# Kernel optimization log

Measured on AMD Instinct MI355X. Metric: run time of the kernel, lower is better.

## Reference

```python
import jax, jax.numpy as jnp
import numpy as np

GRID_SIZE = 5
SPLINE_ORDER = 3
N_COEFFS = GRID_SIZE + SPLINE_ORDER  # 8
N_KNOTS = N_COEFFS + SPLINE_ORDER    # 11
GRID_RANGE = 5.0
# extended knot grid: linspace(-9, 9, 11) for the defaults
_lo = -GRID_RANGE - (SPLINE_ORDER - 1) * 2.0 * GRID_RANGE / GRID_SIZE
_hi = GRID_RANGE + (SPLINE_ORDER - 1) * 2.0 * GRID_RANGE / GRID_SIZE
GRID = jnp.asarray(np.linspace(_lo, _hi, N_KNOTS), dtype=jnp.float32)


def _bspline_basis(x):
    # x: (B, I) -> basis: (B, I, N_COEFFS) via Cox-de Boor recursion
    xe = x[..., None]  # (B, I, 1)
    # order-1 (piecewise-constant) basis over the 10 knot intervals
    bases = ((xe >= GRID[:-1]) & (xe < GRID[1:])).astype(x.dtype)  # (B, I, 10)
    for k in range(1, SPLINE_ORDER):
        n = N_KNOTS - k - 1  # number of bases at this order
        g_i = GRID[:n]
        g_ik = GRID[k:k + n]
        g_i1 = GRID[1:n + 1]
        g_ik1 = GRID[k + 1:k + 1 + n]
        d1 = g_ik - g_i
        d2 = g_ik1 - g_i1
        left = jnp.where(d1 > 1e-8, (xe - g_i) / jnp.where(d1 > 1e-8, d1, 1.0), 0.0) * bases[..., :n]
        right = jnp.where(d2 > 1e-8, (g_ik1 - xe) / jnp.where(d2 > 1e-8, d2, 1.0), 0.0) * bases[..., 1:n + 1]
        bases = left + right
    return bases  # (B, I, 8)


def setup_inputs() -> dict:
    key = jax.random.key(0)
    k1, k2, k3 = jax.random.split(key, 3)
    B, I, O = 8192, 1024, 1024
    x = jax.random.normal(k1, (B, I), dtype=jnp.float32)
    base_weight = jax.random.normal(k2, (O, I), dtype=jnp.float32) * 0.1
    spline_weight = jax.random.normal(k3, (O, I, N_COEFFS), dtype=jnp.float32) * 0.1
    return {"x": x, "base_weight": base_weight, "spline_weight": spline_weight}


def reference(x, base_weight, spline_weight):
    base_out = jnp.einsum('bi,oi->bo', jax.nn.silu(x), base_weight)
    basis = _bspline_basis(x)  # (B, I, 8)
    spline_out = jnp.einsum('bin,oin->bo', basis, spline_weight)
    return base_out + spline_out
```

## Files before the change

### kernel.cpp

```cpp
#include <hip/hip_runtime.h>
#include <hip/hip_bf16.h>

#define B_DIM 8192
#define I_DIM 1024
#define O_DIM 1024
#define K_DIM 9216

#define BM 256
#define BN 128
#define BK 64
#define NKT (K_DIM / BK)

typedef unsigned short ushort_t;
typedef __attribute__((ext_vector_type(8))) short short8;
typedef __attribute__((ext_vector_type(4))) float f32x4;

#define MFMA(a, b, c) __builtin_amdgcn_mfma_f32_16x16x32_bf16((a), (b), (c), 0, 0, 0)

__device__ __forceinline__ ushort_t f2bf(float f) {
    unsigned u = __float_as_uint(f);
    unsigned r = 0x7fffu + ((u >> 16) & 1u);
    return (ushort_t)((u + r) >> 16);
}

__device__ __forceinline__ void llds16(const ushort_t* g, ushort_t* l) {
    __builtin_amdgcn_global_load_lds(
        (const __attribute__((address_space(1))) unsigned int*)g,
        (__attribute__((address_space(3))) unsigned int*)l,
        16, 0, 0);
}

__global__ __launch_bounds__(256) void expand_w_kernel(
        const float* __restrict__ bw, const float* __restrict__ sw,
        ushort_t* __restrict__ Wf) {
    int idx = blockIdx.x * 256 + threadIdx.x;
    int o = idx >> 9;
    int i = (idx & 511) << 1;
    ushort_t* out = Wf + (size_t)o * K_DIM + i;
    const float* bp = bw + ((size_t)o << 10) + i;
    *(unsigned*)out = (unsigned)f2bf(bp[0]) | ((unsigned)f2bf(bp[1]) << 16);
    const float* sp = sw + (((size_t)o << 10) + i) * 8;
    float v[16];
    #pragma unroll
    for (int n = 0; n < 16; ++n) v[n] = sp[n];
    #pragma unroll
    for (int n = 0; n < 8; ++n)
        *(unsigned*)(out + (size_t)(n + 1) * 1024) =
            (unsigned)f2bf(v[n]) | ((unsigned)f2bf(v[8 + n]) << 16);
}

__global__ __launch_bounds__(256) void expand_a_kernel(
        const float* __restrict__ x, ushort_t* __restrict__ Af) {
    int idx = blockIdx.x * 256 + threadIdx.x;
    int b = idx >> 9;
    int i = (idx & 511) << 1;
    const float* xp = x + ((size_t)b << 10) + i;
    float x0 = xp[0], x1 = xp[1];
    ushort_t* out = Af + (size_t)b * K_DIM + i;
    float s0 = x0 / (1.0f + __expf(-x0));
    float s1 = x1 / (1.0f + __expf(-x1));
    *(unsigned*)out = (unsigned)f2bf(s0) | ((unsigned)f2bf(s1) << 16);
    float t0 = (x0 + 9.0f) * (1.0f / 1.8f);
    float t1 = (x1 + 9.0f) * (1.0f / 1.8f);
    float fj0 = floorf(t0), fj1 = floorf(t1);
    int j0 = (int)fj0, j1 = (int)fj1;
    float u0 = t0 - fj0, u1 = t1 - fj1;
    float p0 = 0.5f * (1.f - u0) * (1.f - u0);
    float p1 = 0.5f * (-2.f * u0 * u0 + 2.f * u0 + 1.f);
    float p2 = 0.5f * u0 * u0;
    float q0 = 0.5f * (1.f - u1) * (1.f - u1);
    float q1 = 0.5f * (-2.f * u1 * u1 + 2.f * u1 + 1.f);
    float q2 = 0.5f * u1 * u1;
    #pragma unroll
    for (int n = 0; n < 8; ++n) {
        float v0 = (n == j0 - 2) ? p0 : (n == j0 - 1) ? p1 : (n == j0) ? p2 : 0.f;
        float v1 = (n == j1 - 2) ? q0 : (n == j1 - 1) ? q1 : (n == j1) ? q2 : 0.f;
        *(unsigned*)(out + (size_t)(n + 1) * 1024) =
            (unsigned)f2bf(v0) | ((unsigned)f2bf(v1) << 16);
    }
}

__global__ __launch_bounds__(512, 1) void gemm_bt(
        const ushort_t* __restrict__ Af,
        const ushort_t* __restrict__ Wf,
        float* __restrict__ out) {
    __shared__ __align__(16) ushort_t As[3][BM * BK];
    __shared__ __align__(16) ushort_t Bs[3][BN * BK];

    const int tid = threadIdx.x;

    const int orig = blockIdx.x;
    const int wgid = (orig & 7) * 32 + (orig >> 3);
    const int bm = wgid >> 3;
    const int bn = wgid & 7;
    const int mBase = bm * BM, nBase = bn * BN;

    const int lane = tid & 63;
    const int w = tid >> 6;
    const int wr = (w >> 1) * 64, wc = (w & 1) * 64;
    const int fr = lane & 15;
    const int kg = lane >> 4;

    const int srow = tid >> 3;
    const int scolE = (((tid & 7) ^ (srow & 7)) << 3);
    const int sdst = (tid & ~63) * 8;

    auto stageA = [&](int t, int buf, int rnd) {
        const ushort_t* g = Af + (size_t)(mBase + rnd * 64 + srow) * K_DIM
                               + (size_t)t * BK + scolE;
        llds16(g, &As[buf][rnd * 4096 + sdst]);
    };
    auto stageB = [&](int t, int buf, int rnd) {
        const ushort_t* g = Wf + (size_t)(nBase + rnd * 64 + srow) * K_DIM
                               + (size_t)t * BK + scolE;
        llds16(g, &Bs[buf][rnd * 4096 + sdst]);
    };

    int offA[4][2], offB[4][2];
    #pragma unroll
    for (int m = 0; m < 4; ++m) {
        int row = wr + m * 16 + fr;
        #pragma unroll
        for (int kk = 0; kk < 2; ++kk)
            offA[m][kk] = row * BK + (((kk * 4 + kg) ^ (row & 7)) << 3);
    }
    #pragma unroll
    for (int n = 0; n < 4; ++n) {
        int row = wc + n * 16 + fr;
        #pragma unroll
        for (int kk = 0; kk < 2; ++kk)
            offB[n][kk] = row * BK + (((kk * 4 + kg) ^ (row & 7)) << 3);
    }

    f32x4 acc[4][4];
    #pragma unroll
    for (int m = 0; m < 4; ++m)
        #pragma unroll
        for (int n = 0; n < 4; ++n) acc[m][n] = (f32x4){0.f, 0.f, 0.f, 0.f};

    stageA(0, 0, 0); stageA(0, 0, 1); stageA(0, 0, 2); stageA(0, 0, 3);
    stageB(0, 0, 0); stageB(0, 0, 1);
    stageA(1, 1, 0); stageA(1, 1, 1); stageA(1, 1, 2); stageA(1, 1, 3);
    stageB(1, 1, 0); stageB(1, 1, 1);

    int cur = 0;
    for (int t = 0; t < NKT; ++t) {
        if (t + 1 < NKT) asm volatile("s_waitcnt vmcnt(6)" ::: "memory");
        else             asm volatile("s_waitcnt vmcnt(0)" ::: "memory");
        __builtin_amdgcn_s_barrier();

        const int pf = (cur >= 1) ? cur - 1 : 2;
        const bool dopf = (t + 2 < NKT);
        const ushort_t* A_ = As[cur];
        const ushort_t* B_ = Bs[cur];

        short8 a[4][2], b[2][2];
        #pragma unroll
        for (int m = 0; m < 4; ++m) {
            a[m][0] = *(const short8*)&A_[offA[m][0]];
            a[m][1] = *(const short8*)&A_[offA[m][1]];
        }
        #pragma unroll
        for (int n = 0; n < 2; ++n) {
            b[n][0] = *(const short8*)&B_[offB[n][0]];
            b[n][1] = *(const short8*)&B_[offB[n][1]];
        }
        if (dopf) { stageA(t + 2, pf, 0); stageA(t + 2, pf, 1); stageA(t + 2, pf, 2); }
        asm volatile("s_waitcnt lgkmcnt(0)" ::: "memory");
        __builtin_amdgcn_sched_barrier(0);
        __builtin_amdgcn_s_setprio(1);
        #pragma unroll
        for (int m = 0; m < 4; ++m)
            #pragma unroll
            for (int n = 0; n < 2; ++n) {
                acc[m][n] = MFMA(a[m][0], b[n][0], acc[m][n]);
                acc[m][n] = MFMA(a[m][1], b[n][1], acc[m][n]);
            }
        __builtin_amdgcn_s_setprio(0);
        __builtin_amdgcn_s_barrier();

        short8 b2[2][2];
        #pragma unroll
        for (int n = 0; n < 2; ++n) {
            b2[n][0] = *(const short8*)&B_[offB[2 + n][0]];
            b2[n][1] = *(const short8*)&B_[offB[2 + n][1]];
        }
        if (dopf) { stageA(t + 2, pf, 3); stageB(t + 2, pf, 0); stageB(t + 2, pf, 1); }
        asm volatile("s_waitcnt lgkmcnt(0)" ::: "memory");
        __builtin_amdgcn_sched_barrier(0);
        __builtin_amdgcn_s_setprio(1);
        #pragma unroll
        for (int m = 0; m < 4; ++m)
            #pragma unroll
            for (int n = 0; n < 2; ++n) {
                acc[m][2 + n] = MFMA(a[m][0], b2[n][0], acc[m][2 + n]);
                acc[m][2 + n] = MFMA(a[m][1], b2[n][1], acc[m][2 + n]);
            }
        __builtin_amdgcn_s_setprio(0);

        cur = (cur + 1 == 3) ? 0 : cur + 1;
    }

    const int orow = (lane >> 4) * 4;
    const int ocol = lane & 15;
    #pragma unroll
    for (int m = 0; m < 4; ++m)
        #pragma unroll
        for (int n = 0; n < 4; ++n) {
            size_t base = (size_t)(mBase + wr + m * 16 + orow) * O_DIM
                        + (nBase + wc + n * 16 + ocol);
            #pragma unroll
            for (int r = 0; r < 4; ++r)
                out[base + (size_t)r * O_DIM] = acc[m][n][r];
        }
}

extern "C" void kernel_launch(void* const* d_in, const int* in_sizes, int n_in,
                              void* d_out, int out_size, void* d_ws, size_t ws_size,
                              hipStream_t stream) {
    const float* x  = (const float*)d_in[0];
    const float* bw = (const float*)d_in[1];
    const float* sw = (const float*)d_in[2];
    float* out = (float*)d_out;

    ushort_t* Wf = (ushort_t*)d_ws;
    ushort_t* Af = Wf + (size_t)O_DIM * K_DIM;

    expand_w_kernel<<<(O_DIM * I_DIM / 2) / 256, 256, 0, stream>>>(bw, sw, Wf);
    expand_a_kernel<<<(B_DIM * I_DIM / 2) / 256, 256, 0, stream>>>(x, Af);
    gemm_bt<<<(B_DIM / BM) * (O_DIM / BN), 512, 0, stream>>>(Af, Wf, out);
}
```

Before: 171.5 us.

## Use 256x256 GEMM tiles with split-K over two halves and reduction

Grows the GEMM block tile from 256x128 to 256x256, which raises per-block data reuse and gives each warp 8x4 accumulators. To keep the GPU occupied with fewer tiles, K is split in two when the workspace is large enough. Each split writes a partial result and a separate kernel adds them. The LDS pipeline is reworked to double-buffer B and triple-buffer A, with four MFMA phases per k-tile. The cost is an extra 32MB partial write, a reduction pass, and higher register pressure.

```diff
diff --git a/kernel.cpp b/kernel.cpp
--- a/kernel.cpp
+++ b/kernel.cpp
@@ -7,9 +7,8 @@
 #define K_DIM 9216
 
 #define BM 256
-#define BN 128
+#define BN 256
 #define BK 64
-#define NKT (K_DIM / BK)
 
 typedef unsigned short ushort_t;
 typedef __attribute__((ext_vector_type(8))) short short8;
@@ -83,21 +82,26 @@
 __global__ __launch_bounds__(512, 1) void gemm_bt(
         const ushort_t* __restrict__ Af,
         const ushort_t* __restrict__ Wf,
-        float* __restrict__ out) {
+        float* __restrict__ out, float* __restrict__ part1,
+        int kTiles) {
     __shared__ __align__(16) ushort_t As[3][BM * BK];
-    __shared__ __align__(16) ushort_t Bs[3][BN * BK];
+    __shared__ __align__(16) ushort_t Bs[2][BN * BK];
 
     const int tid = threadIdx.x;
 
+    const int nwg = gridDim.x;
     const int orig = blockIdx.x;
-    const int wgid = (orig & 7) * 32 + (orig >> 3);
-    const int bm = wgid >> 3;
-    const int bn = wgid & 7;
+    const int wgid = (orig & 7) * (nwg >> 3) + (orig >> 3);
+    const int split = wgid >> 7;
+    const int bm = (wgid & 127) >> 2;
+    const int bn = wgid & 3;
     const int mBase = bm * BM, nBase = bn * BN;
+    const size_t kOff = (size_t)split * kTiles * BK;
 
     const int lane = tid & 63;
     const int w = tid >> 6;
-    const int wr = (w >> 1) * 64, wc = (w & 1) * 64;
+    const int wr = (w >> 2) * 128;
+    const int wc = (w & 3) * 64;
     const int fr = lane & 15;
     const int kg = lane >> 4;
 
@@ -107,112 +111,162 @@
 
     auto stageA = [&](int t, int buf, int rnd) {
         const ushort_t* g = Af + (size_t)(mBase + rnd * 64 + srow) * K_DIM
-                               + (size_t)t * BK + scolE;
+                               + kOff + (size_t)t * BK + scolE;
         llds16(g, &As[buf][rnd * 4096 + sdst]);
     };
     auto stageB = [&](int t, int buf, int rnd) {
         const ushort_t* g = Wf + (size_t)(nBase + rnd * 64 + srow) * K_DIM
-                               + (size_t)t * BK + scolE;
+                               + kOff + (size_t)t * BK + scolE;
         llds16(g, &Bs[buf][rnd * 4096 + sdst]);
     };
 
-    int offA[4][2], offB[4][2];
-    #pragma unroll
-    for (int m = 0; m < 4; ++m) {
-        int row = wr + m * 16 + fr;
-        #pragma unroll
-        for (int kk = 0; kk < 2; ++kk)
-            offA[m][kk] = row * BK + (((kk * 4 + kg) ^ (row & 7)) << 3);
-    }
-    #pragma unroll
-    for (int n = 0; n < 4; ++n) {
-        int row = wc + n * 16 + fr;
-        #pragma unroll
-        for (int kk = 0; kk < 2; ++kk)
-            offB[n][kk] = row * BK + (((kk * 4 + kg) ^ (row & 7)) << 3);
-    }
-
-    f32x4 acc[4][4];
-    #pragma unroll
-    for (int m = 0; m < 4; ++m)
+    const int swz0 = ((kg ^ (fr & 7)) << 3);
+    const int swz1 = (((4 + kg) ^ (fr & 7)) << 3);
+
+    f32x4 acc[8][4];
+    #pragma unroll
+    for (int m = 0; m < 8; ++m)
         #pragma unroll
         for (int n = 0; n < 4; ++n) acc[m][n] = (f32x4){0.f, 0.f, 0.f, 0.f};
 
+    stageB(0, 0, 0); stageB(0, 0, 1); stageB(0, 0, 2); stageB(0, 0, 3);
     stageA(0, 0, 0); stageA(0, 0, 1); stageA(0, 0, 2); stageA(0, 0, 3);
-    stageB(0, 0, 0); stageB(0, 0, 1);
     stageA(1, 1, 0); stageA(1, 1, 1); stageA(1, 1, 2); stageA(1, 1, 3);
-    stageB(1, 1, 0); stageB(1, 1, 1);
-
-    int cur = 0;
-    for (int t = 0; t < NKT; ++t) {
-        if (t + 1 < NKT) asm volatile("s_waitcnt vmcnt(6)" ::: "memory");
-        else             asm volatile("s_waitcnt vmcnt(0)" ::: "memory");
+
+    int ca = 0;
+    for (int t = 0; t < kTiles; ++t) {
+        if (t + 1 < kTiles) asm volatile("s_waitcnt vmcnt(4)" ::: "memory");
+        else                asm volatile("s_waitcnt vmcnt(0)" ::: "memory");
         __builtin_amdgcn_s_barrier();
 
-        const int pf = (cur >= 1) ? cur - 1 : 2;
-        const bool dopf = (t + 2 < NKT);
-        const ushort_t* A_ = As[cur];
-        const ushort_t* B_ = Bs[cur];
-
-        short8 a[4][2], b[2][2];
+        const int pa = (ca >= 1) ? ca - 1 : 2;
+        const ushort_t* A_ = As[ca];
+        const ushort_t* B_ = Bs[t & 1];
+
+        if (t + 1 < kTiles) {
+            stageB(t + 1, (t + 1) & 1, 0); stageB(t + 1, (t + 1) & 1, 1);
+            stageB(t + 1, (t + 1) & 1, 2); stageB(t + 1, (t + 1) & 1, 3);
+        }
+        short8 b[4][2];
         #pragma unroll
-        for (int m = 0; m < 4; ++m) {
-            a[m][0] = *(const short8*)&A_[offA[m][0]];
-            a[m][1] = *(const short8*)&A_[offA[m][1]];
-        }
-        #pragma unroll
-        for (int n = 0; n < 2; ++n) {
-            b[n][0] = *(const short8*)&B_[offB[n][0]];
-            b[n][1] = *(const short8*)&B_[offB[n][1]];
-        }
-        if (dopf) { stageA(t + 2, pf, 0); stageA(t + 2, pf, 1); stageA(t + 2, pf, 2); }
-        asm volatile("s_waitcnt lgkmcnt(0)" ::: "memory");
-        __builtin_amdgcn_sched_barrier(0);
-        __builtin_amdgcn_s_setprio(1);
-        #pragma unroll
-        for (int m = 0; m < 4; ++m)
-            #pragma unroll
-            for (int n = 0; n < 2; ++n) {
-                acc[m][n] = MFMA(a[m][0], b[n][0], acc[m][n]);
-                acc[m][n] = MFMA(a[m][1], b[n][1], acc[m][n]);
-            }
-        __builtin_amdgcn_s_setprio(0);
+        for (int n = 0; n < 4; ++n) {
+            int brow = (wc + n * 16 + fr) * BK;
+            b[n][0] = *(const short8*)&B_[brow + swz0];
+            b[n][1] = *(const short8*)&B_[brow + swz1];
+        }
+        {
+            short8 a[2][2];
+            #pragma unroll
+            for (int m = 0; m < 2; ++m) {
+                int arow = (wr + m * 16 + fr) * BK;
+                a[m][0] = *(const short8*)&A_[arow + swz0];
+                a[m][1] = *(const short8*)&A_[arow + swz1];
+            }
+            asm volatile("s_waitcnt lgkmcnt(0)" ::: "memory");
+            __builtin_amdgcn_sched_barrier(0);
+            __builtin_amdgcn_s_setprio(1);
+            #pragma unroll
+            for (int m = 0; m < 2; ++m)
+                #pragma unroll
+                for (int n = 0; n < 4; ++n) {
+                    acc[m][n] = MFMA(a[m][0], b[n][0], acc[m][n]);
+                    acc[m][n] = MFMA(a[m][1], b[n][1], acc[m][n]);
+                }
+            __builtin_amdgcn_s_setprio(0);
+        }
+
+        if (t + 2 < kTiles) {
+            stageA(t + 2, pa, 0); stageA(t + 2, pa, 1);
+            stageA(t + 2, pa, 2); stageA(t + 2, pa, 3);
+        }
+        {
+            short8 a[2][2];
+            #pragma unroll
+            for (int m = 0; m < 2; ++m) {
+                int arow = (wr + (2 + m) * 16 + fr) * BK;
+                a[m][0] = *(const short8*)&A_[arow + swz0];
+                a[m][1] = *(const short8*)&A_[arow + swz1];
+            }
+            asm volatile("s_waitcnt lgkmcnt(0)" ::: "memory");
+            __builtin_amdgcn_sched_barrier(0);
+            __builtin_amdgcn_s_setprio(1);
+            #pragma unroll
+            for (int m = 0; m < 2; ++m)
+                #pragma unroll
+                for (int n = 0; n < 4; ++n) {
+                    acc[2 + m][n] = MFMA(a[m][0], b[n][0], acc[2 + m][n]);
+                    acc[2 + m][n] = MFMA(a[m][1], b[n][1], acc[2 + m][n]);
+                }
+            __builtin_amdgcn_s_setprio(0);
+        }
         __builtin_amdgcn_s_barrier();
 
-        short8 b2[2][2];
-        #pragma unroll
-        for (int n = 0; n < 2; ++n) {
-            b2[n][0] = *(const short8*)&B_[offB[2 + n][0]];
-            b2[n][1] = *(const short8*)&B_[offB[2 + n][1]];
-        }
-        if (dopf) { stageA(t + 2, pf, 3); stageB(t + 2, pf, 0); stageB(t + 2, pf, 1); }
-        asm volatile("s_waitcnt lgkmcnt(0)" ::: "memory");
-        __builtin_amdgcn_sched_barrier(0);
-        __builtin_amdgcn_s_setprio(1);
-        #pragma unroll
-        for (int m = 0; m < 4; ++m)
-            #pragma unroll
-            for (int n = 0; n < 2; ++n) {
-                acc[m][2 + n] = MFMA(a[m][0], b2[n][0], acc[m][2 + n]);
-                acc[m][2 + n] = MFMA(a[m][1], b2[n][1], acc[m][2 + n]);
-            }
-        __builtin_amdgcn_s_setprio(0);
-
-        cur = (cur + 1 == 3) ? 0 : cur + 1;
+        {
+            short8 a[2][2];
+            #pragma unroll
+            for (int m = 0; m < 2; ++m) {
+                int arow = (wr + (4 + m) * 16 + fr) * BK;
+                a[m][0] = *(const short8*)&A_[arow + swz0];
+                a[m][1] = *(const short8*)&A_[arow + swz1];
+            }
+            asm volatile("s_waitcnt lgkmcnt(0)" ::: "memory");
+            __builtin_amdgcn_sched_barrier(0);
+            __builtin_amdgcn_s_setprio(1);
+            #pragma unroll
+            for (int m = 0; m < 2; ++m)
+                #pragma unroll
+                for (int n = 0; n < 4; ++n) {
+                    acc[4 + m][n] = MFMA(a[m][0], b[n][0], acc[4 + m][n]);
+                    acc[4 + m][n] = MFMA(a[m][1], b[n][1], acc[4 + m][n]);
+                }
+            __builtin_amdgcn_s_setprio(0);
+        }
+
+        {
+            short8 a[2][2];
+            #pragma unroll
+            for (int m = 0; m < 2; ++m) {
+                int arow = (wr + (6 + m) * 16 + fr) * BK;
+                a[m][0] = *(const short8*)&A_[arow + swz0];
+                a[m][1] = *(const short8*)&A_[arow + swz1];
+            }
+            asm volatile("s_waitcnt lgkmcnt(0)" ::: "memory");
+            __builtin_amdgcn_sched_barrier(0);
+            __builtin_amdgcn_s_setprio(1);
+            #pragma unroll
+            for (int m = 0; m < 2; ++m)
+                #pragma unroll
+                for (int n = 0; n < 4; ++n) {
+                    acc[6 + m][n] = MFMA(a[m][0], b[n][0], acc[6 + m][n]);
+                    acc[6 + m][n] = MFMA(a[m][1], b[n][1], acc[6 + m][n]);
+                }
+            __builtin_amdgcn_s_setprio(0);
+        }
+
+        ca = (ca + 1 == 3) ? 0 : ca + 1;
     }
 
+    float* obase = split ? part1 : out;
     const int orow = (lane >> 4) * 4;
     const int ocol = lane & 15;
     #pragma unroll
-    for (int m = 0; m < 4; ++m)
+    for (int m = 0; m < 8; ++m)
         #pragma unroll
         for (int n = 0; n < 4; ++n) {
             size_t base = (size_t)(mBase + wr + m * 16 + orow) * O_DIM
                         + (nBase + wc + n * 16 + ocol);
             #pragma unroll
             for (int r = 0; r < 4; ++r)
-                out[base + (size_t)r * O_DIM] = acc[m][n][r];
-        }
+                obase[base + (size_t)r * O_DIM] = acc[m][n][r];
+        }
+}
+
+__global__ __launch_bounds__(256) void reduce_kernel(
+        float* __restrict__ out, const float* __restrict__ p1) {
+    int i = blockIdx.x * 256 + threadIdx.x;
+    f32x4 a = ((const f32x4*)out)[i];
+    f32x4 b = ((const f32x4*)p1)[i];
+    ((f32x4*)out)[i] = a + b;
 }
 
 extern "C" void kernel_launch(void* const* d_in, const int* in_sizes, int n_in,
@@ -223,10 +277,20 @@
     const float* sw = (const float*)d_in[2];
     float* out = (float*)d_out;
 
+    const size_t nW = (size_t)O_DIM * K_DIM;
+    const size_t nA = (size_t)B_DIM * K_DIM;
     ushort_t* Wf = (ushort_t*)d_ws;
-    ushort_t* Af = Wf + (size_t)O_DIM * K_DIM;
+    ushort_t* Af = Wf + nW;
+    float* part1 = (float*)(Af + nA);
+    const size_t need = (nW + nA) * 2 + (size_t)B_DIM * O_DIM * 4;
+
+    const int nsplit = (ws_size >= need) ? 2 : 1;
+    const int kTiles = (K_DIM / BK) / nsplit;
+    const int nwg = 128 * nsplit;
 
     expand_w_kernel<<<(O_DIM * I_DIM / 2) / 256, 256, 0, stream>>>(bw, sw, Wf);
     expand_a_kernel<<<(B_DIM * I_DIM / 2) / 256, 256, 0, stream>>>(x, Af);
-    gemm_bt<<<(B_DIM / BM) * (O_DIM / BN), 512, 0, stream>>>(Af, Wf, out);
-}
+    gemm_bt<<<nwg, 512, 0, stream>>>(Af, Wf, out, part1, kTiles);
+    if (nsplit == 2)
+        reduce_kernel<<<(B_DIM * O_DIM / 4) / 256, 256, 0, stream>>>(out, part1);
+}
```

Result: slower. 220.7 us (+28.7%).

## Load weight tile fragments directly to registers and drop B shared-memory staging

Applied to the files above, without the earlier changes.

The GEMM no longer stages the weight (B) tile through LDS. Each wave loads its B fragments straight from global memory into double-buffered registers one k-tile ahead, while the A tile stays on the triple-buffered global-to-LDS path. The block index mapping also becomes column-major over M, so consecutive blocks share the same weight columns, and the occupancy hint of 1 is dropped from launch bounds. This cuts LDS use and LDS reads, but adds register pressure and makes uncoalesced 16-byte global loads for B that depend on cache hits.

```diff
diff --git a/kernel.cpp b/kernel.cpp
--- a/kernel.cpp
+++ b/kernel.cpp
@@ -80,19 +80,18 @@
     }
 }
 
-__global__ __launch_bounds__(512, 1) void gemm_bt(
+__global__ __launch_bounds__(512) void gemm_bt(
         const ushort_t* __restrict__ Af,
         const ushort_t* __restrict__ Wf,
         float* __restrict__ out) {
     __shared__ __align__(16) ushort_t As[3][BM * BK];
-    __shared__ __align__(16) ushort_t Bs[3][BN * BK];
 
     const int tid = threadIdx.x;
 
     const int orig = blockIdx.x;
     const int wgid = (orig & 7) * 32 + (orig >> 3);
-    const int bm = wgid >> 3;
-    const int bn = wgid & 7;
+    const int bn = wgid >> 5;
+    const int bm = wgid & 31;
     const int mBase = bm * BM, nBase = bn * BN;
 
     const int lane = tid & 63;
@@ -105,32 +104,27 @@
     const int scolE = (((tid & 7) ^ (srow & 7)) << 3);
     const int sdst = (tid & ~63) * 8;
 
-    auto stageA = [&](int t, int buf, int rnd) {
-        const ushort_t* g = Af + (size_t)(mBase + rnd * 64 + srow) * K_DIM
-                               + (size_t)t * BK + scolE;
-        llds16(g, &As[buf][rnd * 4096 + sdst]);
+    auto stageA = [&](int t, int buf) {
+        #pragma unroll
+        for (int rnd = 0; rnd < 4; ++rnd) {
+            const ushort_t* g = Af + (size_t)(mBase + rnd * 64 + srow) * K_DIM
+                                   + (size_t)t * BK + scolE;
+            llds16(g, &As[buf][rnd * 4096 + sdst]);
+        }
     };
-    auto stageB = [&](int t, int buf, int rnd) {
-        const ushort_t* g = Wf + (size_t)(nBase + rnd * 64 + srow) * K_DIM
-                               + (size_t)t * BK + scolE;
-        llds16(g, &Bs[buf][rnd * 4096 + sdst]);
+
+    const ushort_t* Wbase = Wf + (size_t)(nBase + wc + fr) * K_DIM + kg * 8;
+    auto bload = [&](int t, short8 (&b)[4][2]) {
+        #pragma unroll
+        for (int n = 0; n < 4; ++n)
+            #pragma unroll
+            for (int kk = 0; kk < 2; ++kk)
+                b[n][kk] = *(const short8*)(Wbase + (size_t)n * 16 * K_DIM
+                                                  + (size_t)t * BK + kk * 32);
     };
 
-    int offA[4][2], offB[4][2];
-    #pragma unroll
-    for (int m = 0; m < 4; ++m) {
-        int row = wr + m * 16 + fr;
-        #pragma unroll
-        for (int kk = 0; kk < 2; ++kk)
-            offA[m][kk] = row * BK + (((kk * 4 + kg) ^ (row & 7)) << 3);
-    }
-    #pragma unroll
-    for (int n = 0; n < 4; ++n) {
-        int row = wc + n * 16 + fr;
-        #pragma unroll
-        for (int kk = 0; kk < 2; ++kk)
-            offB[n][kk] = row * BK + (((kk * 4 + kg) ^ (row & 7)) << 3);
-    }
+    const int swz0 = ((kg ^ (fr & 7)) << 3);
+    const int swz1 = (((4 + kg) ^ (fr & 7)) << 3);
 
     f32x4 acc[4][4];
     #pragma unroll
@@ -138,67 +132,71 @@
         #pragma unroll
         for (int n = 0; n < 4; ++n) acc[m][n] = (f32x4){0.f, 0.f, 0.f, 0.f};
 
-    stageA(0, 0, 0); stageA(0, 0, 1); stageA(0, 0, 2); stageA(0, 0, 3);
-    stageB(0, 0, 0); stageB(0, 0, 1);
-    stageA(1, 1, 0); stageA(1, 1, 1); stageA(1, 1, 2); stageA(1, 1, 3);
-    stageB(1, 1, 0); stageB(1, 1, 1);
-
-    int cur = 0;
-    for (int t = 0; t < NKT; ++t) {
-        if (t + 1 < NKT) asm volatile("s_waitcnt vmcnt(6)" ::: "memory");
-        else             asm volatile("s_waitcnt vmcnt(0)" ::: "memory");
+    short8 bA[4][2], bB[4][2];
+
+    bload(0, bA);
+    __builtin_amdgcn_sched_barrier(0);
+    stageA(0, 0);
+    stageA(1, 1);
+
+    int ca = 0;
+    auto tile = [&](int t, short8 (&bc)[4][2], short8 (&bnx)[4][2]) {
+        if (t == NKT - 1) asm volatile("s_waitcnt vmcnt(0)" ::: "memory");
+        else              asm volatile("s_waitcnt vmcnt(4)" ::: "memory");
         __builtin_amdgcn_s_barrier();
 
-        const int pf = (cur >= 1) ? cur - 1 : 2;
-        const bool dopf = (t + 2 < NKT);
-        const ushort_t* A_ = As[cur];
-        const ushort_t* B_ = Bs[cur];
-
-        short8 a[4][2], b[2][2];
-        #pragma unroll
-        for (int m = 0; m < 4; ++m) {
-            a[m][0] = *(const short8*)&A_[offA[m][0]];
-            a[m][1] = *(const short8*)&A_[offA[m][1]];
-        }
-        #pragma unroll
-        for (int n = 0; n < 2; ++n) {
-            b[n][0] = *(const short8*)&B_[offB[n][0]];
-            b[n][1] = *(const short8*)&B_[offB[n][1]];
-        }
-        if (dopf) { stageA(t + 2, pf, 0); stageA(t + 2, pf, 1); stageA(t + 2, pf, 2); }
+        const ushort_t* A_ = As[ca];
+        const int pa = (ca >= 1) ? ca - 1 : 2;
+
+        if (t + 1 < NKT) bload(t + 1, bnx);
+        __builtin_amdgcn_sched_barrier(0);
+        short8 a1[2][2];
+        #pragma unroll
+        for (int i = 0; i < 2; ++i) {
+            int arow = (wr + i * 16 + fr) * BK;
+            a1[i][0] = *(const short8*)&A_[arow + swz0];
+            a1[i][1] = *(const short8*)&A_[arow + swz1];
+        }
         asm volatile("s_waitcnt lgkmcnt(0)" ::: "memory");
         __builtin_amdgcn_sched_barrier(0);
         __builtin_amdgcn_s_setprio(1);
         #pragma unroll
-        for (int m = 0; m < 4; ++m)
-            #pragma unroll
-            for (int n = 0; n < 2; ++n) {
-                acc[m][n] = MFMA(a[m][0], b[n][0], acc[m][n]);
-                acc[m][n] = MFMA(a[m][1], b[n][1], acc[m][n]);
+        for (int i = 0; i < 2; ++i)
+            #pragma unroll
+            for (int n = 0; n < 4; ++n) {
+                acc[i][n] = MFMA(a1[i][0], bc[n][0], acc[i][n]);
+                acc[i][n] = MFMA(a1[i][1], bc[n][1], acc[i][n]);
             }
         __builtin_amdgcn_s_setprio(0);
         __builtin_amdgcn_s_barrier();
 
-        short8 b2[2][2];
-        #pragma unroll
-        for (int n = 0; n < 2; ++n) {
-            b2[n][0] = *(const short8*)&B_[offB[2 + n][0]];
-            b2[n][1] = *(const short8*)&B_[offB[2 + n][1]];
-        }
-        if (dopf) { stageA(t + 2, pf, 3); stageB(t + 2, pf, 0); stageB(t + 2, pf, 1); }
+        if (t + 2 < NKT) stageA(t + 2, pa);
+        __builtin_amdgcn_sched_barrier(0);
+        short8 a2[2][2];
+        #pragma unroll
+        for (int i = 0; i < 2; ++i) {
+            int arow = (wr + (2 + i) * 16 + fr) * BK;
+            a2[i][0] = *(const short8*)&A_[arow + swz0];
+            a2[i][1] = *(const short8*)&A_[arow + swz1];
+        }
         asm volatile("s_waitcnt lgkmcnt(0)" ::: "memory");
         __builtin_amdgcn_sched_barrier(0);
         __builtin_amdgcn_s_setprio(1);
         #pragma unroll
-        for (int m = 0; m < 4; ++m)
-            #pragma unroll
-            for (int n = 0; n < 2; ++n) {
-                acc[m][2 + n] = MFMA(a[m][0], b2[n][0], acc[m][2 + n]);
-                acc[m][2 + n] = MFMA(a[m][1], b2[n][1], acc[m][2 + n]);
+        for (int i = 0; i < 2; ++i)
+            #pragma unroll
+            for (int n = 0; n < 4; ++n) {
+                acc[2 + i][n] = MFMA(a2[i][0], bc[n][0], acc[2 + i][n]);
+                acc[2 + i][n] = MFMA(a2[i][1], bc[n][1], acc[2 + i][n]);
             }
         __builtin_amdgcn_s_setprio(0);
 
-        cur = (cur + 1 == 3) ? 0 : cur + 1;
+        ca = (ca + 1 == 3) ? 0 : ca + 1;
+    };
+
+    for (int t = 0; t < NKT; t += 2) {
+        tile(t, bA, bB);
+        tile(t + 1, bB, bA);
     }
 
     const int orow = (lane >> 4) * 4;
```

After: 408.0 us. 138% more time.

## Shrink GEMM tile to 128x128 with 256 threads, double-buffer, two blocks per CU

Applied to the files above, without the earlier changes.

The GEMM drops from 256x128 tiles with 512 threads and a triple-buffered LDS ring to 128x128 tiles with 256 threads and double buffering. The launch bounds now allow two workgroups per CU, and the grid doubles to 512 blocks. Each k-step issues the next A-tile prefetch before the first MFMA half and the B prefetch before the second half, then waits for vmcnt(0) at the top of every step. This aims to raise occupancy and balance the workload across CUs, at the cost of less data reuse per tile, more global traffic, and a shallower prefetch pipeline.

```diff
diff --git a/kernel.cpp b/kernel.cpp
--- a/kernel.cpp
+++ b/kernel.cpp
@@ -6,7 +6,7 @@
 #define O_DIM 1024
 #define K_DIM 9216
 
-#define BM 256
+#define BM 128
 #define BN 128
 #define BK 64
 #define NKT (K_DIM / BK)
@@ -80,17 +80,17 @@
     }
 }
 
-__global__ __launch_bounds__(512, 1) void gemm_bt(
+__global__ __launch_bounds__(256, 2) void gemm_bt(
         const ushort_t* __restrict__ Af,
         const ushort_t* __restrict__ Wf,
         float* __restrict__ out) {
-    __shared__ __align__(16) ushort_t As[3][BM * BK];
-    __shared__ __align__(16) ushort_t Bs[3][BN * BK];
+    __shared__ __align__(16) ushort_t As[2][BM * BK];
+    __shared__ __align__(16) ushort_t Bs[2][BN * BK];
 
     const int tid = threadIdx.x;
 
     const int orig = blockIdx.x;
-    const int wgid = (orig & 7) * 32 + (orig >> 3);
+    const int wgid = (orig & 7) * 64 + (orig >> 3);
     const int bm = wgid >> 3;
     const int bn = wgid & 7;
     const int mBase = bm * BM, nBase = bn * BN;
@@ -103,34 +103,27 @@
 
     const int srow = tid >> 3;
     const int scolE = (((tid & 7) ^ (srow & 7)) << 3);
-    const int sdst = (tid & ~63) * 8;
-
-    auto stageA = [&](int t, int buf, int rnd) {
-        const ushort_t* g = Af + (size_t)(mBase + rnd * 64 + srow) * K_DIM
-                               + (size_t)t * BK + scolE;
-        llds16(g, &As[buf][rnd * 4096 + sdst]);
+    const int sdst = (tid >> 6) * 512;
+
+    auto stageA = [&](int t, int buf) {
+        #pragma unroll
+        for (int rnd = 0; rnd < 4; ++rnd) {
+            const ushort_t* g = Af + (size_t)(mBase + rnd * 32 + srow) * K_DIM
+                                   + (size_t)t * BK + scolE;
+            llds16(g, &As[buf][rnd * 2048 + sdst]);
+        }
     };
-    auto stageB = [&](int t, int buf, int rnd) {
-        const ushort_t* g = Wf + (size_t)(nBase + rnd * 64 + srow) * K_DIM
-                               + (size_t)t * BK + scolE;
-        llds16(g, &Bs[buf][rnd * 4096 + sdst]);
+    auto stageB = [&](int t, int buf) {
+        #pragma unroll
+        for (int rnd = 0; rnd < 4; ++rnd) {
+            const ushort_t* g = Wf + (size_t)(nBase + rnd * 32 + srow) * K_DIM
+                                   + (size_t)t * BK + scolE;
+            llds16(g, &Bs[buf][rnd * 2048 + sdst]);
+        }
     };
 
-    int offA[4][2], offB[4][2];
-    #pragma unroll
-    for (int m = 0; m < 4; ++m) {
-        int row = wr + m * 16 + fr;
-        #pragma unroll
-        for (int kk = 0; kk < 2; ++kk)
-            offA[m][kk] = row * BK + (((kk * 4 + kg) ^ (row & 7)) << 3);
-    }
-    #pragma unroll
-    for (int n = 0; n < 4; ++n) {
-        int row = wc + n * 16 + fr;
-        #pragma unroll
-        for (int kk = 0; kk < 2; ++kk)
-            offB[n][kk] = row * BK + (((kk * 4 + kg) ^ (row & 7)) << 3);
-    }
+    const int swz0 = ((kg ^ (fr & 7)) << 3);
+    const int swz1 = (((4 + kg) ^ (fr & 7)) << 3);
 
     f32x4 acc[4][4];
     #pragma unroll
@@ -138,34 +131,32 @@
         #pragma unroll
         for (int n = 0; n < 4; ++n) acc[m][n] = (f32x4){0.f, 0.f, 0.f, 0.f};
 
-    stageA(0, 0, 0); stageA(0, 0, 1); stageA(0, 0, 2); stageA(0, 0, 3);
-    stageB(0, 0, 0); stageB(0, 0, 1);
-    stageA(1, 1, 0); stageA(1, 1, 1); stageA(1, 1, 2); stageA(1, 1, 3);
-    stageB(1, 1, 0); stageB(1, 1, 1);
-
-    int cur = 0;
+    stageA(0, 0);
+    stageB(0, 0);
+
     for (int t = 0; t < NKT; ++t) {
-        if (t + 1 < NKT) asm volatile("s_waitcnt vmcnt(6)" ::: "memory");
-        else             asm volatile("s_waitcnt vmcnt(0)" ::: "memory");
+        const int cur = t & 1, nb = cur ^ 1;
+        asm volatile("s_waitcnt vmcnt(0)" ::: "memory");
         __builtin_amdgcn_s_barrier();
 
-        const int pf = (cur >= 1) ? cur - 1 : 2;
-        const bool dopf = (t + 2 < NKT);
         const ushort_t* A_ = As[cur];
         const ushort_t* B_ = Bs[cur];
 
-        short8 a[4][2], b[2][2];
+        if (t + 1 < NKT) stageA(t + 1, nb);
+        __builtin_amdgcn_sched_barrier(0);
+        short8 a[4][2], b0[2][2], b1[2][2];
         #pragma unroll
         for (int m = 0; m < 4; ++m) {
-            a[m][0] = *(const short8*)&A_[offA[m][0]];
-            a[m][1] = *(const short8*)&A_[offA[m][1]];
+            int arow = (wr + m * 16 + fr) * BK;
+            a[m][0] = *(const short8*)&A_[arow + swz0];
+            a[m][1] = *(const short8*)&A_[arow + swz1];
         }
         #pragma unroll
         for (int n = 0; n < 2; ++n) {
-            b[n][0] = *(const short8*)&B_[offB[n][0]];
-            b[n][1] = *(const short8*)&B_[offB[n][1]];
-        }
-        if (dopf) { stageA(t + 2, pf, 0); stageA(t + 2, pf, 1); stageA(t + 2, pf, 2); }
+            int brow = (wc + n * 16 + fr) * BK;
+            b0[n][0] = *(const short8*)&B_[brow + swz0];
+            b0[n][1] = *(const short8*)&B_[brow + swz1];
+        }
         asm volatile("s_waitcnt lgkmcnt(0)" ::: "memory");
         __builtin_amdgcn_sched_barrier(0);
         __builtin_amdgcn_s_setprio(1);
@@ -173,19 +164,20 @@
         for (int m = 0; m < 4; ++m)
             #pragma unroll
             for (int n = 0; n < 2; ++n) {
-                acc[m][n] = MFMA(a[m][0], b[n][0], acc[m][n]);
-                acc[m][n] = MFMA(a[m][1], b[n][1], acc[m][n]);
+                acc[m][n] = MFMA(a[m][0], b0[n][0], acc[m][n]);
+                acc[m][n] = MFMA(a[m][1], b0[n][1], acc[m][n]);
             }
         __builtin_amdgcn_s_setprio(0);
         __builtin_amdgcn_s_barrier();
 
-        short8 b2[2][2];
+        if (t + 1 < NKT) stageB(t + 1, nb);
+        __builtin_amdgcn_sched_barrier(0);
         #pragma unroll
         for (int n = 0; n < 2; ++n) {
-            b2[n][0] = *(const short8*)&B_[offB[2 + n][0]];
-            b2[n][1] = *(const short8*)&B_[offB[2 + n][1]];
-        }
-        if (dopf) { stageA(t + 2, pf, 3); stageB(t + 2, pf, 0); stageB(t + 2, pf, 1); }
+            int brow = (wc + (2 + n) * 16 + fr) * BK;
+            b1[n][0] = *(const short8*)&B_[brow + swz0];
+            b1[n][1] = *(const short8*)&B_[brow + swz1];
+        }
         asm volatile("s_waitcnt lgkmcnt(0)" ::: "memory");
         __builtin_amdgcn_sched_barrier(0);
         __builtin_amdgcn_s_setprio(1);
@@ -193,12 +185,10 @@
         for (int m = 0; m < 4; ++m)
             #pragma unroll
             for (int n = 0; n < 2; ++n) {
-                acc[m][2 + n] = MFMA(a[m][0], b2[n][0], acc[m][2 + n]);
-                acc[m][2 + n] = MFMA(a[m][1], b2[n][1], acc[m][2 + n]);
+                acc[m][2 + n] = MFMA(a[m][0], b1[n][0], acc[m][2 + n]);
+                acc[m][2 + n] = MFMA(a[m][1], b1[n][1], acc[m][2 + n]);
             }
         __builtin_amdgcn_s_setprio(0);
-
-        cur = (cur + 1 == 3) ? 0 : cur + 1;
     }
 
     const int orow = (lane >> 4) * 4;
@@ -228,5 +218,5 @@
 
     expand_w_kernel<<<(O_DIM * I_DIM / 2) / 256, 256, 0, stream>>>(bw, sw, Wf);
     expand_a_kernel<<<(B_DIM * I_DIM / 2) / 256, 256, 0, stream>>>(x, Af);
-    gemm_bt<<<(B_DIM / BM) * (O_DIM / BN), 512, 0, stream>>>(Af, Wf, out);
-}
+    gemm_bt<<<(B_DIM / BM) * (O_DIM / BN), 256, 0, stream>>>(Af, Wf, out);
+}
```

Result: slower. 234.4 us (+36.7%).
